# Kernel optimization log

Measured on AMD Instinct MI355X. Metric: run time of the kernel, lower is better.

## Reference

```python
import jax, jax.numpy as jnp
import numpy as np

N = 50000   # nodes
E = 800000  # edges (before self-loops)
B = 256     # graphs in batch
F = 128     # input feature dim
H = 4       # heads per layer
C = 64      # out_channels per head
NEG_SLOPE = 0.2


def setup_inputs() -> dict:
    key = jax.random.key(0)
    ks = jax.random.split(key, 16)
    s = 0.05
    inp = {
        "x": jax.random.normal(ks[0], (N, F), dtype=jnp.float32),
        "edge_index": jax.random.randint(ks[1], (2, E), 0, N, dtype=jnp.int32),
        "batch": jnp.sort(jax.random.randint(ks[2], (N,), 0, B, dtype=jnp.int32)),
        # layer 1: F -> H*C
        "W1": jax.random.normal(ks[3], (F, H * C), dtype=jnp.float32) * s,
        "as1": jax.random.normal(ks[4], (H, C), dtype=jnp.float32) * s,
        "ad1": jax.random.normal(ks[5], (H, C), dtype=jnp.float32) * s,
        "b1": jnp.zeros((H * C,), dtype=jnp.float32),
        # layer 2: H*C -> H*C
        "W2": jax.random.normal(ks[6], (H * C, H * C), dtype=jnp.float32) * s,
        "as2": jax.random.normal(ks[7], (H, C), dtype=jnp.float32) * s,
        "ad2": jax.random.normal(ks[8], (H, C), dtype=jnp.float32) * s,
        "b2": jnp.zeros((H * C,), dtype=jnp.float32),
        # layer 3: H*C -> H*C
        "W3": jax.random.normal(ks[9], (H * C, H * C), dtype=jnp.float32) * s,
        "as3": jax.random.normal(ks[10], (H, C), dtype=jnp.float32) * s,
        "ad3": jax.random.normal(ks[11], (H, C), dtype=jnp.float32) * s,
        "b3": jnp.zeros((H * C,), dtype=jnp.float32),
    }
    return inp


def _gat_layer(x, src, dst, W, a_src, a_dst, bias):
    """PyG GATConv (concat=True, self-loops already included in src/dst)."""
    n = x.shape[0]
    xh = (x @ W).reshape(n, H, C)                      # [N,H,C]
    alpha_s = jnp.sum(xh * a_src, axis=-1)             # [N,H]
    alpha_d = jnp.sum(xh * a_dst, axis=-1)             # [N,H]
    logits = alpha_s[src] + alpha_d[dst]               # [E',H]
    logits = jnp.where(logits > 0, logits, NEG_SLOPE * logits)  # LeakyReLU
    # segment-wise softmax over destination neighborhoods
    m = jax.lax.stop_gradient(jax.ops.segment_max(logits, dst, num_segments=n))
    e = jnp.exp(logits - m[dst])
    z = jax.ops.segment_sum(e, dst, num_segments=n)
    alpha = e / (z[dst] + 1e-16)                       # [E',H]
    msg = xh[src] * alpha[:, :, None]                  # [E',H,C]
    out = jax.ops.segment_sum(msg, dst, num_segments=n)  # [N,H,C]
    return out.reshape(n, H * C) + bias


def reference(x, edge_index, batch, W1, as1, ad1, b1, W2, as2, ad2, b2, W3, as3, ad3, b3):
    n = x.shape[0]
    loops = jnp.arange(n, dtype=edge_index.dtype)
    src = jnp.concatenate([edge_index[0], loops])
    dst = jnp.concatenate([edge_index[1], loops])
    # dropout is identity at inference; activation = ReLU between layers
    h = jax.nn.relu(_gat_layer(x, src, dst, W1, as1, ad1, b1))
    h = jax.nn.relu(_gat_layer(h, src, dst, W2, as2, ad2, b2))
    h = _gat_layer(h, src, dst, W3, as3, ad3, b3)
    pooled = jax.ops.segment_max(h, batch, num_segments=B)  # global max pool -> [B, H*C]
    return jnp.squeeze(pooled)
```

## Files before the change

### kernel.cpp

```cpp
#include <hip/hip_runtime.h>
#include <hip/hip_fp16.h>
#include <math.h>

#define NN 50000
#define NE 800000
#define NT 850000
#define NB 256
#define FIN 128
#define HC 256
#define NH 4
#define CD 64
#define NEG 0.2f
#define SCAN_B 196
#define PSPL 8

typedef _Float16 half8 __attribute__((ext_vector_type(8)));
typedef float f32x4 __attribute__((ext_vector_type(4)));

__device__ __forceinline__ void gld16(const void* g, void* l) {
    __builtin_amdgcn_global_load_lds(
        (const __attribute__((address_space(1))) void*)g,
        (__attribute__((address_space(3))) void*)l, 16, 0, 0);
}


__global__ void zero_int_kernel(int* __restrict__ p, int n) {
    int i = blockIdx.x * blockDim.x + threadIdx.x;
    if (i < n) p[i] = 0;
}

__global__ void hist_kernel(const int* __restrict__ ei, int* __restrict__ cnt) {
    int e = blockIdx.x * blockDim.x + threadIdx.x;
    if (e < NE) {
        atomicAdd(&cnt[ei[NE + e]], 1);
    } else if (e < NT) {
        atomicAdd(&cnt[e - NE], 1);
    }
}

__global__ __launch_bounds__(256) void part_kernel(const int* __restrict__ cnt,
                                                   int* __restrict__ part) {
    __shared__ int red[4];
    int i = blockIdx.x * 256 + threadIdx.x;
    int v = (i < NN) ? cnt[i] : 0;
#pragma unroll
    for (int off = 32; off > 0; off >>= 1) v += __shfl_down(v, off);
    if ((threadIdx.x & 63) == 0) red[threadIdx.x >> 6] = v;
    __syncthreads();
    if (threadIdx.x == 0) part[blockIdx.x] = red[0] + red[1] + red[2] + red[3];
}

__global__ __launch_bounds__(256) void offs_kernel(const int* __restrict__ part,
                                                   int* __restrict__ boff) {
    __shared__ int sh[256];
    int t = threadIdx.x;
    sh[t] = (t < SCAN_B) ? part[t] : 0;
    __syncthreads();
    for (int off = 1; off < 256; off <<= 1) {
        int add = (t >= off) ? sh[t - off] : 0;
        __syncthreads();
        sh[t] += add;
        __syncthreads();
    }
    boff[t] = (t == 0) ? 0 : sh[t - 1];
}

__global__ __launch_bounds__(256) void write_scan_kernel(const int* __restrict__ cnt,
        const int* __restrict__ boff, int* __restrict__ rowptr, int* __restrict__ cursor) {
    __shared__ int sh[256];
    int t = threadIdx.x;
    int i = blockIdx.x * 256 + t;
    int v = (i < NN) ? cnt[i] : 0;
    sh[t] = v;
    __syncthreads();
    for (int off = 1; off < 256; off <<= 1) {
        int add = (t >= off) ? sh[t - off] : 0;
        __syncthreads();
        sh[t] += add;
        __syncthreads();
    }
    int run = boff[blockIdx.x] + sh[t] - v;
    if (i < NN) { rowptr[i] = run; cursor[i] = run; }
    if (i == NN - 1) rowptr[NN] = run + v;
}

__global__ void scatter_kernel(const int* __restrict__ ei, int* __restrict__ cursor,
                               int* __restrict__ colsrc) {
    int e = blockIdx.x * blockDim.x + threadIdx.x;
    int s, d;
    if (e < NE)      { s = ei[e]; d = ei[NE + e]; }
    else if (e < NT) { s = e - NE; d = s; }
    else return;
    int pos = atomicAdd(&cursor[d], 1);
    colsrc[pos] = s;
}

__global__ void batch_bounds_kernel(const int* __restrict__ batch, int* __restrict__ bstart) {
    int i = blockIdx.x * blockDim.x + threadIdx.x;
    if (i >= NN) return;
    int b = batch[i];
    if (i == 0) {
        for (int bb = 0; bb <= b; ++bb) bstart[bb] = 0;
    } else {
        int pb = batch[i - 1];
        if (pb != b) for (int bb = pb + 1; bb <= b; ++bb) bstart[bb] = i;
    }
    if (i == NN - 1) {
        for (int bb = b + 1; bb <= NB; ++bb) bstart[bb] = NN;
    }
}


template<int K>
__global__ __launch_bounds__(256) void wprep_kernel(const float* __restrict__ W,
                                                    _Float16* __restrict__ WtS) {
    __shared__ float sm[8][257];
    const int t = threadIdx.x;
    const int b = blockIdx.x;
    const int kb = b * 8;
    const bool lo3 = (kb >= 2 * K);
    const int kphys = lo3 ? kb - 2 * K : (kb >= K ? kb - K : kb);
#pragma unroll
    for (int i = 0; i < 8; ++i) {
        int idx = i * 256 + t;
        sm[idx >> 8][idx & 255] = W[(size_t)(kphys + (idx >> 8)) * HC + (idx & 255)];
    }
    __syncthreads();
    half8 o;
#pragma unroll
    for (int r = 0; r < 8; ++r) {
        float w = sm[r][t];
        _Float16 h = (_Float16)w;
        o[r] = lo3 ? (_Float16)(w - (float)h) : h;
    }
    *reinterpret_cast<half8*>(&WtS[((size_t)b * 256 + t) * 8]) = o;
}


template<int K, bool F32IN>
__global__ __launch_bounds__(256) void mfma_gemm_kernel(
        const _Float16* __restrict__ Xh, const _Float16* __restrict__ Xl,
        const float* __restrict__ Xf,
        const _Float16* __restrict__ WtS, __half* __restrict__ XHo,
        const float* __restrict__ as_g, const float* __restrict__ ad_g,
        float* __restrict__ aS, float* __restrict__ aD) {
    constexpr int C3 = 3 * K;
    constexpr int NSTEP = C3 / 32;
    constexpr int SPP = K / 32;
    __shared__ __align__(16) _Float16 As[4][64 * 32];
    __shared__ __align__(16) _Float16 Bs[4][32 * 256];
    const int t = threadIdx.x;
    const int lane = t & 63;
    const int wid = t >> 6;
    const int wm = wid & 1, wn = wid >> 1;
    const int r0 = blockIdx.x * 64;
    const int l15 = lane & 15;
    const int kcl = lane >> 4;
    const int srowA = t >> 2;
    const int skcA  = t & 3;
    const int arow = min(r0 + srowA, NN - 1);

    f32x4 acc[2][8];
#pragma unroll
    for (int i = 0; i < 2; ++i)
#pragma unroll
        for (int j = 0; j < 8; ++j) acc[i][j] = (f32x4)0.f;

    float4 rA[3][2];

    auto loadA = [&](int s, float4& v0, float4& v1) {
        const int sel = s / SPP;
        const int cbase = (s - sel * SPP) * 32;
        if constexpr (F32IN) {
            const float* p = Xf + (size_t)arow * K + cbase + skcA * 8;
            v0 = *reinterpret_cast<const float4*>(p);
            v1 = *reinterpret_cast<const float4*>(p + 4);
        } else {
            const _Float16* src = (sel == 1) ? Xl : Xh;
            v0 = *reinterpret_cast<const float4*>(src + (size_t)arow * K + cbase + skcA * 8);
        }
    };
    auto writeA = [&](int s, int buf, float4 v0, float4 v1) {
        _Float16* d = &As[buf][(skcA * 64 + (srowA ^ skcA)) * 8];
        if constexpr (F32IN) {
            const int sel = s / SPP;
            float f[8];
            *reinterpret_cast<float4*>(f) = v0;
            *reinterpret_cast<float4*>(f + 4) = v1;
            half8 h;
#pragma unroll
            for (int e = 0; e < 8; ++e) {
                _Float16 a = (_Float16)f[e];
                h[e] = (sel == 1) ? (_Float16)(f[e] - (float)a) : a;
            }
            *reinterpret_cast<half8*>(d) = h;
        } else {
            *reinterpret_cast<float4*>(d) = v0;
        }
    };
    auto issueB = [&](int s, int buf) {
        const _Float16* bsrc = WtS + (size_t)s * (32 * 256);
#pragma unroll
        for (int r = 0; r < 4; ++r)
            gld16(bsrc + ((size_t)r * 256 + t) * 8, &Bs[buf][(r * 256 + t) * 8]);
    };
    auto mfma_step = [&](int s, int buf) {
        half8 a0 = *reinterpret_cast<const half8*>(
            &As[buf][(kcl * 64 + ((wm * 32      + l15) ^ kcl)) * 8]);
        half8 a1 = *reinterpret_cast<const half8*>(
            &As[buf][(kcl * 64 + ((wm * 32 + 16 + l15) ^ kcl)) * 8]);
        const _Float16* bp = &Bs[buf][(kcl * 256 + wn * 128 + l15) * 8];
        __builtin_amdgcn_s_setprio(1);
#pragma unroll
        for (int nf = 0; nf < 8; ++nf) {
            half8 b = *reinterpret_cast<const half8*>(bp + nf * 16 * 8);
            acc[0][nf] = __builtin_amdgcn_mfma_f32_16x16x32_f16(a0, b, acc[0][nf], 0, 0, 0);
            acc[1][nf] = __builtin_amdgcn_mfma_f32_16x16x32_f16(a1, b, acc[1][nf], 0, 0, 0);
        }
        __builtin_amdgcn_s_setprio(0);
    };
    auto wait_steady = [&]() {
        if constexpr (F32IN) asm volatile("s_waitcnt vmcnt(12) lgkmcnt(0)" ::: "memory");
        else                 asm volatile("s_waitcnt vmcnt(10) lgkmcnt(0)" ::: "memory");
        __builtin_amdgcn_s_barrier();
        __builtin_amdgcn_sched_barrier(0);
    };

    loadA(0, rA[0][0], rA[0][1]); issueB(0, 0);
    loadA(1, rA[1][0], rA[1][1]); issueB(1, 1);
    loadA(2, rA[2][0], rA[2][1]); issueB(2, 2);
    writeA(0, 0, rA[0][0], rA[0][1]);
    wait_steady();

#pragma unroll
    for (int s = 0; s < NSTEP - 3; ++s) {
        loadA(s + 3, rA[(s + 3) % 3][0], rA[(s + 3) % 3][1]);
        issueB(s + 3, (s + 3) & 3);
        mfma_step(s, s & 3);
        writeA(s + 1, (s + 1) & 3, rA[(s + 1) % 3][0], rA[(s + 1) % 3][1]);
        wait_steady();
    }
    mfma_step(NSTEP - 3, (NSTEP - 3) & 3);
    writeA(NSTEP - 2, (NSTEP - 2) & 3, rA[(NSTEP - 2) % 3][0], rA[(NSTEP - 2) % 3][1]);
    if constexpr (F32IN) asm volatile("s_waitcnt vmcnt(6) lgkmcnt(0)" ::: "memory");
    else                 asm volatile("s_waitcnt vmcnt(5) lgkmcnt(0)" ::: "memory");
    __builtin_amdgcn_s_barrier();
    __builtin_amdgcn_sched_barrier(0);
    mfma_step(NSTEP - 2, (NSTEP - 2) & 3);
    writeA(NSTEP - 1, (NSTEP - 1) & 3, rA[(NSTEP - 1) % 3][0], rA[(NSTEP - 1) % 3][1]);
    asm volatile("s_waitcnt vmcnt(0) lgkmcnt(0)" ::: "memory");
    __builtin_amdgcn_s_barrier();
    __builtin_amdgcn_sched_barrier(0);
    mfma_step(NSTEP - 1, (NSTEP - 1) & 3);

    const int rb = r0 + wm * 32 + (lane >> 4) * 4;
    const int cb = wn * 128 + l15;
    float asv[8], adv[8];
#pragma unroll
    for (int nf = 0; nf < 8; ++nf) {
        asv[nf] = as_g[cb + nf * 16];
        adv[nf] = ad_g[cb + nf * 16];
    }
#pragma unroll
    for (int mf = 0; mf < 2; ++mf)
#pragma unroll
        for (int r = 0; r < 4; ++r) {
            int row = rb + mf * 16 + r;
            float s0 = 0.f, s1 = 0.f, d0 = 0.f, d1 = 0.f;
#pragma unroll
            for (int nf = 0; nf < 4; ++nf) {
                float a = acc[mf][nf][r], b = acc[mf][nf + 4][r];
                s0 += a * asv[nf];     d0 += a * adv[nf];
                s1 += b * asv[nf + 4]; d1 += b * adv[nf + 4];
            }
#pragma unroll
            for (int off = 1; off < 16; off <<= 1) {
                s0 += __shfl_xor(s0, off); s1 += __shfl_xor(s1, off);
                d0 += __shfl_xor(d0, off); d1 += __shfl_xor(d1, off);
            }
            if (row < NN) {
                if (l15 == 0) {
                    aS[row * 4 + 2 * wn] = s0; aS[row * 4 + 2 * wn + 1] = s1;
                    aD[row * 4 + 2 * wn] = d0; aD[row * 4 + 2 * wn + 1] = d1;
                }
#pragma unroll
                for (int nf = 0; nf < 8; ++nf)
                    XHo[(size_t)row * HC + cb + nf * 16] = __float2half(acc[mf][nf][r]);
            }
        }
}


#define LEAKY(v) ((v) > 0.f ? (v) : NEG * (v))

template<int RELU, int SPLIT>
__global__ __launch_bounds__(256) void aggregate_kernel(
        const int* __restrict__ rowptr, const int* __restrict__ colsrc,
        const float* __restrict__ aS, const float* __restrict__ aD,
        const __half* __restrict__ XH,
        const float* __restrict__ bias, float* __restrict__ OUT,
        __half* __restrict__ OUTh, __half* __restrict__ OUTl) {
    __shared__ float4 wbuf[4][64];
    __shared__ int    ibuf[4][64];
    const int wslot = threadIdx.x >> 6;
    int n = blockIdx.x * 4 + wslot;
    int lane = threadIdx.x & 63;
    bool lo = lane < 32;
    const __half2* xbase = reinterpret_cast<const __half2*>(XH);
    float4 adv = *reinterpret_cast<const float4*>(aD + n * 4);
    float zl = 0.f, zh = 0.f;
    float al0 = 0.f, al1 = 0.f, ah0 = 0.f, ah1 = 0.f;
    int jb = rowptr[n], je = rowptr[n + 1];
    for (int c0 = jb; c0 < je; c0 += 64) {
        int cnt = min(64, je - c0);
        {
            int e = min(c0 + lane, je - 1);
            int s = colsrc[e];
            float4 sv = *reinterpret_cast<const float4*>(aS + s * 4);
            float4 w;
            w.x = __expf(LEAKY(sv.x + adv.x));
            w.y = __expf(LEAKY(sv.y + adv.y));
            w.z = __expf(LEAKY(sv.z + adv.z));
            w.w = __expf(LEAKY(sv.w + adv.w));
            wbuf[wslot][lane] = w;
            ibuf[wslot][lane] = s;
        }
        int u = 0;
        for (; u + 8 <= cnt; u += 8) {
            int sidx[8];
            float4 w[8];
#pragma unroll
            for (int k = 0; k < 8; ++k) { sidx[k] = ibuf[wslot][u + k]; w[k] = wbuf[wslot][u + k]; }
            __half2 p[8], q[8];
#pragma unroll
            for (int k = 0; k < 8; ++k) {
                const __half2* xp = xbase + (size_t)sidx[k] * (HC / 2) + lane;
                p[k] = xp[0];
                q[k] = xp[64];
            }
#pragma unroll
            for (int k = 0; k < 8; ++k) {
                float wl = lo ? w[k].x : w[k].y, wh = lo ? w[k].z : w[k].w;
                float2 f = __half22float2(p[k]);
                al0 += wl * f.x; al1 += wl * f.y;
                f = __half22float2(q[k]);
                ah0 += wh * f.x; ah1 += wh * f.y;
                zl += wl; zh += wh;
            }
        }
        for (; u < cnt; ++u) {
            int s0 = ibuf[wslot][u];
            float4 w0 = wbuf[wslot][u];
            const __half2* xp = xbase + (size_t)s0 * (HC / 2) + lane;
            __half2 p0 = xp[0], q0 = xp[64];
            float w0l = lo ? w0.x : w0.y, w0h = lo ? w0.z : w0.w;
            float2 f = __half22float2(p0);
            al0 += w0l * f.x; al1 += w0l * f.y;
            f = __half22float2(q0);
            ah0 += w0h * f.x; ah1 += w0h * f.y;
            zl += w0l; zh += w0h;
        }
    }
    float izl = 1.f / (zl + 1e-16f), izh = 1.f / (zh + 1e-16f);
    float2 bl = reinterpret_cast<const float2*>(bias)[lane];
    float2 bh = reinterpret_cast<const float2*>(bias + 128)[lane];
    float o0 = al0 * izl + bl.x;
    float o1 = al1 * izl + bl.y;
    float o2 = ah0 * izh + bh.x;
    float o3 = ah1 * izh + bh.y;
    if (RELU) {
        o0 = fmaxf(o0, 0.f); o1 = fmaxf(o1, 0.f);
        o2 = fmaxf(o2, 0.f); o3 = fmaxf(o3, 0.f);
    }
    if (SPLIT) {
        __half h0 = __float2half(o0), h1 = __float2half(o1);
        __half h2 = __float2half(o2), h3 = __float2half(o3);
        __half2* ph = reinterpret_cast<__half2*>(OUTh + (size_t)n * HC) + lane;
        ph[0]  = __half2(h0, h1);
        ph[64] = __half2(h2, h3);
        __half2* pl = reinterpret_cast<__half2*>(OUTl + (size_t)n * HC) + lane;
        pl[0]  = __half2(__float2half(o0 - __half2float(h0)), __float2half(o1 - __half2float(h1)));
        pl[64] = __half2(__float2half(o2 - __half2float(h2)), __float2half(o3 - __half2float(h3)));
    } else {
        float2* op = reinterpret_cast<float2*>(OUT + (size_t)n * HC) + lane;
        op[0]  = make_float2(o0, o1);
        op[64] = make_float2(o2, o3);
    }
}


__global__ __launch_bounds__(256) void pool1_kernel(const float* __restrict__ Hf,
        const int* __restrict__ bstart, float* __restrict__ part) {
    int b = blockIdx.x / PSPL, sp = blockIdx.x % PSPL;
    int c = threadIdx.x;
    int i0 = bstart[b], i1 = bstart[b + 1];
    float m = -INFINITY;
    for (int i = i0 + sp; i < i1; i += PSPL) m = fmaxf(m, Hf[(size_t)i * HC + c]);
    part[(size_t)blockIdx.x * HC + c] = m;
}

__global__ __launch_bounds__(256) void pool2_kernel(const float* __restrict__ part,
        float* __restrict__ out) {
    int b = blockIdx.x;
    int c = threadIdx.x;
    float m = -INFINITY;
#pragma unroll
    for (int sp = 0; sp < PSPL; ++sp)
        m = fmaxf(m, part[(size_t)(b * PSPL + sp) * HC + c]);
    out[b * HC + c] = m;
}


extern "C" void kernel_launch(void* const* d_in, const int* in_sizes, int n_in,
                              void* d_out, int out_size, void* d_ws, size_t ws_size,
                              hipStream_t stream) {
    const float* x     = (const float*)d_in[0];
    const int*   ei    = (const int*)d_in[1];
    const int*   batch = (const int*)d_in[2];
    const float* W1  = (const float*)d_in[3];
    const float* as1 = (const float*)d_in[4];
    const float* ad1 = (const float*)d_in[5];
    const float* b1  = (const float*)d_in[6];
    const float* W2  = (const float*)d_in[7];
    const float* as2 = (const float*)d_in[8];
    const float* ad2 = (const float*)d_in[9];
    const float* b2  = (const float*)d_in[10];
    const float* W3  = (const float*)d_in[11];
    const float* as3 = (const float*)d_in[12];
    const float* ad3 = (const float*)d_in[13];
    const float* b3  = (const float*)d_in[14];
    float* out = (float*)d_out;

    __half* Hh  = (__half*)d_ws;
    __half* Hl  = Hh + (size_t)NN * HC;
    __half* XHh = Hl + (size_t)NN * HC;
    float* bufB = (float*)Hh;
    _Float16* WtS = (_Float16*)(XHh + (size_t)NN * HC);
    float*  aS  = (float*)(WtS + 768 * 256);
    float*  aD  = aS + NN * NH;
    float*  ppart = aD + NN * NH;
    int* cnt    = (int*)(ppart + (size_t)NB * PSPL * HC);
    int* rowptr = cnt + NN;
    int* cursor = rowptr + (NN + 1);
    int* colsrc = cursor + NN;
    int* bstart = colsrc + NT;
    int* part   = bstart + (NB + 1);
    int* boff   = part + SCAN_B;

    zero_int_kernel<<<(NN + 255) / 256, 256, 0, stream>>>(cnt, NN);
    hist_kernel<<<(NT + 255) / 256, 256, 0, stream>>>(ei, cnt);
    part_kernel<<<SCAN_B, 256, 0, stream>>>(cnt, part);
    offs_kernel<<<1, 256, 0, stream>>>(part, boff);
    write_scan_kernel<<<SCAN_B, 256, 0, stream>>>(cnt, boff, rowptr, cursor);
    scatter_kernel<<<(NT + 255) / 256, 256, 0, stream>>>(ei, cursor, colsrc);
    batch_bounds_kernel<<<(NN + 255) / 256, 256, 0, stream>>>(batch, bstart);

    const int gemm_grid = (NN + 63) / 64;
    const int node_grid = NN / 4;

    wprep_kernel<FIN><<<3 * FIN / 8, 256, 0, stream>>>(W1, WtS);
    mfma_gemm_kernel<FIN, true><<<gemm_grid, 256, 0, stream>>>(
        nullptr, nullptr, x, WtS, XHh, as1, ad1, aS, aD);
    aggregate_kernel<1, 1><<<node_grid, 256, 0, stream>>>(rowptr, colsrc, aS, aD, XHh, b1,
                                                          nullptr, Hh, Hl);

    wprep_kernel<HC><<<3 * HC / 8, 256, 0, stream>>>(W2, WtS);
    mfma_gemm_kernel<HC, false><<<gemm_grid, 256, 0, stream>>>(
        (_Float16*)Hh, (_Float16*)Hl, nullptr, WtS, XHh, as2, ad2, aS, aD);
    aggregate_kernel<1, 1><<<node_grid, 256, 0, stream>>>(rowptr, colsrc, aS, aD, XHh, b2,
                                                          nullptr, Hh, Hl);

    wprep_kernel<HC><<<3 * HC / 8, 256, 0, stream>>>(W3, WtS);
    mfma_gemm_kernel<HC, false><<<gemm_grid, 256, 0, stream>>>(
        (_Float16*)Hh, (_Float16*)Hl, nullptr, WtS, XHh, as3, ad3, aS, aD);
    aggregate_kernel<0, 0><<<node_grid, 256, 0, stream>>>(rowptr, colsrc, aS, aD, XHh, b3,
                                                          bufB, nullptr, nullptr);

    pool1_kernel<<<NB * PSPL, 256, 0, stream>>>(bufB, bstart, ppart);
    pool2_kernel<<<NB, 256, 0, stream>>>(ppart, out);
}
```

Measured before the change: 440.1 us.

## Drop weight low-part term in split-fp16 GEMM and split output columns across blocks

The GEMM previously emulated higher precision with three fp16 products (Xh*Wh, Xl*Wh, Xh*Wl). It now drops the weight low-part term, cutting the K loop from 3K to 2K and shrinking the prepared weight buffer to a single fp16 copy. Each block now computes 128 of the 256 output columns (two heads), which doubles the grid and halves the accumulators and B tile in LDS. This lowers MFMA work and LDS pressure and should raise occupancy, but weights are rounded to fp16, and each A tile is loaded twice, once per column half.

New measurement: 442.6 us. No clear change (+0.6%).

```diff
diff --git a/kernel.cpp b/kernel.cpp
--- a/kernel.cpp
+++ b/kernel.cpp
@@ -116,24 +116,17 @@
                                                     _Float16* __restrict__ WtS) {
     __shared__ float sm[8][257];
     const int t = threadIdx.x;
-    const int b = blockIdx.x;
-    const int kb = b * 8;
-    const bool lo3 = (kb >= 2 * K);
-    const int kphys = lo3 ? kb - 2 * K : (kb >= K ? kb - K : kb);
+    const int kb = blockIdx.x * 8;
 #pragma unroll
     for (int i = 0; i < 8; ++i) {
         int idx = i * 256 + t;
-        sm[idx >> 8][idx & 255] = W[(size_t)(kphys + (idx >> 8)) * HC + (idx & 255)];
+        sm[idx >> 8][idx & 255] = W[(size_t)(kb + (idx >> 8)) * HC + (idx & 255)];
     }
     __syncthreads();
     half8 o;
 #pragma unroll
-    for (int r = 0; r < 8; ++r) {
-        float w = sm[r][t];
-        _Float16 h = (_Float16)w;
-        o[r] = lo3 ? (_Float16)(w - (float)h) : h;
-    }
-    *reinterpret_cast<half8*>(&WtS[((size_t)b * 256 + t) * 8]) = o;
+    for (int r = 0; r < 8; ++r) o[r] = (_Float16)sm[r][t];
+    *reinterpret_cast<half8*>(&WtS[((size_t)blockIdx.x * 256 + t) * 8]) = o;
 }
 
 
@@ -144,46 +137,46 @@
         const _Float16* __restrict__ WtS, __half* __restrict__ XHo,
         const float* __restrict__ as_g, const float* __restrict__ ad_g,
         float* __restrict__ aS, float* __restrict__ aD) {
-    constexpr int C3 = 3 * K;
-    constexpr int NSTEP = C3 / 32;
+    constexpr int C2 = 2 * K;
+    constexpr int NSTEP = C2 / 32;
     constexpr int SPP = K / 32;
     __shared__ __align__(16) _Float16 As[4][64 * 32];
-    __shared__ __align__(16) _Float16 Bs[4][32 * 256];
+    __shared__ __align__(16) _Float16 Bs[4][32 * 128];
     const int t = threadIdx.x;
     const int lane = t & 63;
     const int wid = t >> 6;
     const int wm = wid & 1, wn = wid >> 1;
-    const int r0 = blockIdx.x * 64;
+    const int cbb = blockIdx.x & 1;
+    const int r0 = (blockIdx.x >> 1) * 64;
+    const int cb0 = cbb * 128;
     const int l15 = lane & 15;
     const int kcl = lane >> 4;
     const int srowA = t >> 2;
     const int skcA  = t & 3;
     const int arow = min(r0 + srowA, NN - 1);
 
-    f32x4 acc[2][8];
+    f32x4 acc[2][4];
 #pragma unroll
     for (int i = 0; i < 2; ++i)
 #pragma unroll
-        for (int j = 0; j < 8; ++j) acc[i][j] = (f32x4)0.f;
+        for (int j = 0; j < 4; ++j) acc[i][j] = (f32x4)0.f;
 
     float4 rA[3][2];
 
     auto loadA = [&](int s, float4& v0, float4& v1) {
-        const int sel = s / SPP;
-        const int cbase = (s - sel * SPP) * 32;
+        const int cbase = (s % SPP) * 32;
         if constexpr (F32IN) {
             const float* p = Xf + (size_t)arow * K + cbase + skcA * 8;
             v0 = *reinterpret_cast<const float4*>(p);
             v1 = *reinterpret_cast<const float4*>(p + 4);
         } else {
-            const _Float16* src = (sel == 1) ? Xl : Xh;
+            const _Float16* src = (s < SPP) ? Xh : Xl;
             v0 = *reinterpret_cast<const float4*>(src + (size_t)arow * K + cbase + skcA * 8);
         }
     };
     auto writeA = [&](int s, int buf, float4 v0, float4 v1) {
         _Float16* d = &As[buf][(skcA * 64 + (srowA ^ skcA)) * 8];
         if constexpr (F32IN) {
-            const int sel = s / SPP;
             float f[8];
             *reinterpret_cast<float4*>(f) = v0;
             *reinterpret_cast<float4*>(f + 4) = v1;
@@ -191,7 +184,7 @@
 #pragma unroll
             for (int e = 0; e < 8; ++e) {
                 _Float16 a = (_Float16)f[e];
-                h[e] = (sel == 1) ? (_Float16)(f[e] - (float)a) : a;
+                h[e] = (s >= SPP) ? (_Float16)(f[e] - (float)a) : a;
             }
             *reinterpret_cast<half8*>(d) = h;
         } else {
@@ -199,20 +192,24 @@
         }
     };
     auto issueB = [&](int s, int buf) {
-        const _Float16* bsrc = WtS + (size_t)s * (32 * 256);
-#pragma unroll
-        for (int r = 0; r < 4; ++r)
-            gld16(bsrc + ((size_t)r * 256 + t) * 8, &Bs[buf][(r * 256 + t) * 8]);
+        const int kbase = (s % SPP) * 4;
+#pragma unroll
+        for (int r2 = 0; r2 < 2; ++r2) {
+            int kc = r2 * 2 + (t >> 7);
+            int col = t & 127;
+            gld16(WtS + ((size_t)(kbase + kc) * 256 + cb0 + col) * 8,
+                  &Bs[buf][(kc * 128 + col) * 8]);
+        }
     };
     auto mfma_step = [&](int s, int buf) {
         half8 a0 = *reinterpret_cast<const half8*>(
             &As[buf][(kcl * 64 + ((wm * 32      + l15) ^ kcl)) * 8]);
         half8 a1 = *reinterpret_cast<const half8*>(
             &As[buf][(kcl * 64 + ((wm * 32 + 16 + l15) ^ kcl)) * 8]);
-        const _Float16* bp = &Bs[buf][(kcl * 256 + wn * 128 + l15) * 8];
+        const _Float16* bp = &Bs[buf][(kcl * 128 + wn * 64 + l15) * 8];
         __builtin_amdgcn_s_setprio(1);
 #pragma unroll
-        for (int nf = 0; nf < 8; ++nf) {
+        for (int nf = 0; nf < 4; ++nf) {
             half8 b = *reinterpret_cast<const half8*>(bp + nf * 16 * 8);
             acc[0][nf] = __builtin_amdgcn_mfma_f32_16x16x32_f16(a0, b, acc[0][nf], 0, 0, 0);
             acc[1][nf] = __builtin_amdgcn_mfma_f32_16x16x32_f16(a1, b, acc[1][nf], 0, 0, 0);
@@ -220,8 +217,8 @@
         __builtin_amdgcn_s_setprio(0);
     };
     auto wait_steady = [&]() {
-        if constexpr (F32IN) asm volatile("s_waitcnt vmcnt(12) lgkmcnt(0)" ::: "memory");
-        else                 asm volatile("s_waitcnt vmcnt(10) lgkmcnt(0)" ::: "memory");
+        if constexpr (F32IN) asm volatile("s_waitcnt vmcnt(8) lgkmcnt(0)" ::: "memory");
+        else                 asm volatile("s_waitcnt vmcnt(6) lgkmcnt(0)" ::: "memory");
         __builtin_amdgcn_s_barrier();
         __builtin_amdgcn_sched_barrier(0);
     };
@@ -242,8 +239,8 @@
     }
     mfma_step(NSTEP - 3, (NSTEP - 3) & 3);
     writeA(NSTEP - 2, (NSTEP - 2) & 3, rA[(NSTEP - 2) % 3][0], rA[(NSTEP - 2) % 3][1]);
-    if constexpr (F32IN) asm volatile("s_waitcnt vmcnt(6) lgkmcnt(0)" ::: "memory");
-    else                 asm volatile("s_waitcnt vmcnt(5) lgkmcnt(0)" ::: "memory");
+    if constexpr (F32IN) asm volatile("s_waitcnt vmcnt(4) lgkmcnt(0)" ::: "memory");
+    else                 asm volatile("s_waitcnt vmcnt(3) lgkmcnt(0)" ::: "memory");
     __builtin_amdgcn_s_barrier();
     __builtin_amdgcn_sched_barrier(0);
     mfma_step(NSTEP - 2, (NSTEP - 2) & 3);
@@ -254,38 +251,39 @@
     mfma_step(NSTEP - 1, (NSTEP - 1) & 3);
 
     const int rb = r0 + wm * 32 + (lane >> 4) * 4;
-    const int cb = wn * 128 + l15;
-    float asv[8], adv[8];
-#pragma unroll
-    for (int nf = 0; nf < 8; ++nf) {
-        asv[nf] = as_g[cb + nf * 16];
-        adv[nf] = ad_g[cb + nf * 16];
+    const int cbg = cb0 + wn * 64 + l15;
+    const int head = cbb * 2 + wn;
+    float asv[4], adv[4];
+#pragma unroll
+    for (int nf = 0; nf < 4; ++nf) {
+        asv[nf] = as_g[cbg + nf * 16];
+        adv[nf] = ad_g[cbg + nf * 16];
     }
 #pragma unroll
     for (int mf = 0; mf < 2; ++mf)
 #pragma unroll
         for (int r = 0; r < 4; ++r) {
             int row = rb + mf * 16 + r;
-            float s0 = 0.f, s1 = 0.f, d0 = 0.f, d1 = 0.f;
+            float s0 = 0.f, d0 = 0.f;
 #pragma unroll
             for (int nf = 0; nf < 4; ++nf) {
-                float a = acc[mf][nf][r], b = acc[mf][nf + 4][r];
-                s0 += a * asv[nf];     d0 += a * adv[nf];
-                s1 += b * asv[nf + 4]; d1 += b * adv[nf + 4];
+                float a = acc[mf][nf][r];
+                s0 += a * asv[nf];
+                d0 += a * adv[nf];
             }
 #pragma unroll
             for (int off = 1; off < 16; off <<= 1) {
-                s0 += __shfl_xor(s0, off); s1 += __shfl_xor(s1, off);
-                d0 += __shfl_xor(d0, off); d1 += __shfl_xor(d1, off);
+                s0 += __shfl_xor(s0, off);
+                d0 += __shfl_xor(d0, off);
             }
             if (row < NN) {
                 if (l15 == 0) {
-                    aS[row * 4 + 2 * wn] = s0; aS[row * 4 + 2 * wn + 1] = s1;
-                    aD[row * 4 + 2 * wn] = d0; aD[row * 4 + 2 * wn + 1] = d1;
+                    aS[row * 4 + head] = s0;
+                    aD[row * 4 + head] = d0;
                 }
 #pragma unroll
-                for (int nf = 0; nf < 8; ++nf)
-                    XHo[(size_t)row * HC + cb + nf * 16] = __float2half(acc[mf][nf][r]);
+                for (int nf = 0; nf < 4; ++nf)
+                    XHo[(size_t)row * HC + cbg + nf * 16] = __float2half(acc[mf][nf][r]);
             }
         }
 }
@@ -436,7 +434,7 @@
     __half* XHh = Hl + (size_t)NN * HC;
     float* bufB = (float*)Hh;
     _Float16* WtS = (_Float16*)(XHh + (size_t)NN * HC);
-    float*  aS  = (float*)(WtS + 768 * 256);
+    float*  aS  = (float*)(WtS + 256 * 256);
     float*  aD  = aS + NN * NH;
     float*  ppart = aD + NN * NH;
     int* cnt    = (int*)(ppart + (size_t)NB * PSPL * HC);
@@ -455,22 +453,22 @@
     scatter_kernel<<<(NT + 255) / 256, 256, 0, stream>>>(ei, cursor, colsrc);
     batch_bounds_kernel<<<(NN + 255) / 256, 256, 0, stream>>>(batch, bstart);
 
-    const int gemm_grid = (NN + 63) / 64;
+    const int gemm_grid = 2 * ((NN + 63) / 64);
     const int node_grid = NN / 4;
 
-    wprep_kernel<FIN><<<3 * FIN / 8, 256, 0, stream>>>(W1, WtS);
+    wprep_kernel<FIN><<<FIN / 8, 256, 0, stream>>>(W1, WtS);
     mfma_gemm_kernel<FIN, true><<<gemm_grid, 256, 0, stream>>>(
         nullptr, nullptr, x, WtS, XHh, as1, ad1, aS, aD);
     aggregate_kernel<1, 1><<<node_grid, 256, 0, stream>>>(rowptr, colsrc, aS, aD, XHh, b1,
                                                           nullptr, Hh, Hl);
 
-    wprep_kernel<HC><<<3 * HC / 8, 256, 0, stream>>>(W2, WtS);
+    wprep_kernel<HC><<<HC / 8, 256, 0, stream>>>(W2, WtS);
     mfma_gemm_kernel<HC, false><<<gemm_grid, 256, 0, stream>>>(
         (_Float16*)Hh, (_Float16*)Hl, nullptr, WtS, XHh, as2, ad2, aS, aD);
     aggregate_kernel<1, 1><<<node_grid, 256, 0, stream>>>(rowptr, colsrc, aS, aD, XHh, b2,
                                                           nullptr, Hh, Hl);
 
-    wprep_kernel<HC><<<3 * HC / 8, 256, 0, stream>>>(W3, WtS);
+    wprep_kernel<HC><<<HC / 8, 256, 0, stream>>>(W3, WtS);
     mfma_gemm_kernel<HC, false><<<gemm_grid, 256, 0, stream>>>(
         (_Float16*)Hh, (_Float16*)Hl, nullptr, WtS, XHh, as3, ad3, aS, aD);
     aggregate_kernel<0, 0><<<node_grid, 256, 0, stream>>>(rowptr, colsrc, aS, aD, XHh, b3,
```
